# Kernel optimization log

Hardware: AMD Instinct MI355X
Metric: run time of the kernel (lower is better)

## Reference

```python
import jax, jax.numpy as jnp
import numpy as np

N, K, F_IN, F_HID, F_OUT = 500000, 16, 7, 40, 3

def setup_inputs() -> dict:
    key = jax.random.key(0)
    k1, k2, k3 = jax.random.split(key, 3)
    mailbox = jax.random.normal(k1, (N, K, F_IN), dtype=jnp.float32)
    W1 = jax.random.normal(k2, (F_IN, F_HID), dtype=jnp.float32) * (1.0 / np.sqrt(F_IN))
    b1 = jnp.zeros((F_HID,), dtype=jnp.float32)
    W2 = jax.random.normal(k3, (F_HID, F_OUT), dtype=jnp.float32) * (1.0 / np.sqrt(F_HID))
    b2 = jnp.zeros((F_OUT,), dtype=jnp.float32)
    return {"mailbox": mailbox, "W1": W1, "b1": b1, "W2": W2, "b2": b2}

def reference(mailbox, W1, b1, W2, b2):
    # MLP 7->40->3 applied per (node, neighbor) message, then mean over neighbors.
    h = jax.nn.relu(jnp.einsum('nkf,fh->nkh', mailbox, W1) + b1)  # [N,K,40]
    y = jnp.einsum('nkh,ho->nko', h, W2) + b2                     # [N,K,3]
    return jnp.mean(y, axis=1)                                    # [N,3]
```

## Files before the change

kernel.cpp:

```cpp
#include <hip/hip_runtime.h>
#include <stdint.h>

#define N_NODES 500000
#define K_NB 16
#define F_IN 7
#define F_HID 40
#define F_OUT 3
#define NODE_FLOATS (K_NB * F_IN)
#define NPW 16
#define WPB 4
#define NPB (NPW * WPB)

typedef __attribute__((address_space(3))) void lds_void_t;
typedef __attribute__((address_space(1))) const void glb_void_t;

__global__ __launch_bounds__(256) void aggre_kernel(
    const float* __restrict__ mailbox,
    const float* __restrict__ W1,
    const float* __restrict__ b1,
    const float* __restrict__ W2,
    const float* __restrict__ b2,
    float* __restrict__ out)
{
    __shared__ float4 w1lds[F_HID * 2];
    __shared__ float4 w2lds[F_HID];
    __shared__ __align__(16) float tile[WPB][NPW * NODE_FLOATS];

    const int t = threadIdx.x;
    if (t < F_HID * 2) {
        const int h = t >> 1;
        float4 v;
        if ((t & 1) == 0) {
            v.x = W1[0 * F_HID + h]; v.y = W1[1 * F_HID + h];
            v.z = W1[2 * F_HID + h]; v.w = W1[3 * F_HID + h];
        } else {
            v.x = W1[4 * F_HID + h]; v.y = W1[5 * F_HID + h];
            v.z = W1[6 * F_HID + h]; v.w = b1[h];
        }
        w1lds[t] = v;
    } else if (t < F_HID * 3) {
        const int h = t - F_HID * 2;
        float4 v;
        v.x = W2[h * F_OUT + 0];
        v.y = W2[h * F_OUT + 1];
        v.z = W2[h * F_OUT + 2];
        v.w = 0.0f;
        w2lds[h] = v;
    }
    __syncthreads();

    const int wave = t >> 6;
    const int lane = t & 63;
    const long tile0 = (long)blockIdx.x * NPB + (long)wave * NPW;
    if (tile0 >= N_NODES) return;

    const float* gsrc = mailbox + (size_t)tile0 * NODE_FLOATS;
    #pragma unroll
    for (int j = 0; j < 7; ++j) {
        const float* g = gsrc + (size_t)(j * 64 + lane) * 4;
        __builtin_amdgcn_global_load_lds(
            (glb_void_t*)g,
            (lds_void_t*)&tile[wave][j * 256],
            16, 0, 0);
    }
    __builtin_amdgcn_s_waitcnt(0x0f70);

    const int nloc = lane >> 2;
    const int r = lane & 3;
    const float* mp = &tile[wave][nloc * NODE_FLOATS + r * 28];
    float m[28];
    #pragma unroll
    for (int i = 0; i < 7; ++i) {
        const float4 v = ((const float4*)mp)[i];
        m[4 * i + 0] = v.x; m[4 * i + 1] = v.y;
        m[4 * i + 2] = v.z; m[4 * i + 3] = v.w;
    }

    float a0 = 0.0f, a1 = 0.0f, a2 = 0.0f;
    #pragma unroll 2
    for (int h = 0; h < F_HID; ++h) {
        const float4 wa = w1lds[2 * h + 0];
        const float4 wb = w1lds[2 * h + 1];
        float sh = 0.0f;
        #pragma unroll
        for (int kk = 0; kk < 4; ++kk) {
            const int o = kk * F_IN;
            float acc = wb.w;
            acc = fmaf(m[o + 0], wa.x, acc);
            acc = fmaf(m[o + 1], wa.y, acc);
            acc = fmaf(m[o + 2], wa.z, acc);
            acc = fmaf(m[o + 3], wa.w, acc);
            acc = fmaf(m[o + 4], wb.x, acc);
            acc = fmaf(m[o + 5], wb.y, acc);
            acc = fmaf(m[o + 6], wb.z, acc);
            sh += fmaxf(acc, 0.0f);
        }
        const float4 w2v = w2lds[h];
        a0 = fmaf(sh, w2v.x, a0);
        a1 = fmaf(sh, w2v.y, a1);
        a2 = fmaf(sh, w2v.z, a2);
    }

    a0 += __shfl_xor(a0, 1); a0 += __shfl_xor(a0, 2);
    a1 += __shfl_xor(a1, 1); a1 += __shfl_xor(a1, 2);
    a2 += __shfl_xor(a2, 1); a2 += __shfl_xor(a2, 2);

    if (r < F_OUT) {
        const float val = (r == 0) ? a0 : ((r == 1) ? a1 : a2);
        out[(size_t)(tile0 + nloc) * F_OUT + r] =
            fmaf(val, 1.0f / (float)K_NB, b2[r]);
    }
}

extern "C" void kernel_launch(void* const* d_in, const int* in_sizes, int n_in,
                              void* d_out, int out_size, void* d_ws, size_t ws_size,
                              hipStream_t stream) {
    const float* mailbox = (const float*)d_in[0];
    const float* W1      = (const float*)d_in[1];
    const float* b1      = (const float*)d_in[2];
    const float* W2      = (const float*)d_in[3];
    const float* b2      = (const float*)d_in[4];
    float* out = (float*)d_out;

    const int blocks = (N_NODES + NPB - 1) / NPB;
    aggre_kernel<<<blocks, 256, 0, stream>>>(mailbox, W1, b1, W2, b2, out);
}
```

Measured before the change: 315.4 us.

## Use packed v2f FMA math with a pre-duplicated weight table from a prep kernel

Adds a small prep kernel that writes W1, b1 and W2 into a workspace table, with each weight duplicated into float pairs. The main kernel reads these pairs through uniform global loads instead of staging weights in LDS behind a block barrier. The per-neighbor MLP is rewritten with two-wide vector FMAs so the compiler can emit packed FP32 instructions, processing two neighbors per operation and roughly halving VALU instruction count. The costs are an extra kernel launch, scalar-stride LDS reads for the messages, and weight reads that may become scalar or vector memory loads.

```diff
diff --git a/kernel.cpp b/kernel.cpp
--- a/kernel.cpp
+++ b/kernel.cpp
@@ -11,44 +11,53 @@
 #define WPB 4
 #define NPB (NPW * WPB)
 
+typedef float v2f __attribute__((ext_vector_type(2)));
+
 typedef __attribute__((address_space(3))) void lds_void_t;
 typedef __attribute__((address_space(1))) const void glb_void_t;
 
+__global__ void prep_kernel(const float* __restrict__ W1,
+                            const float* __restrict__ b1,
+                            const float* __restrict__ W2,
+                            const float* __restrict__ b2,
+                            float* __restrict__ ws)
+{
+    const int t = threadIdx.x;
+    if (t < F_HID) {
+        const int h = t;
+        float* p = ws + h * 16;
+        #pragma unroll
+        for (int i = 0; i < F_IN; ++i) {
+            const float w = W1[i * F_HID + h];
+            p[2 * i + 0] = w;
+            p[2 * i + 1] = w;
+        }
+        p[14] = b1[h];
+        p[15] = b1[h];
+    } else if (t < 2 * F_HID) {
+        const int h = t - F_HID;
+        float* p = ws + 40 * 16 + h * 8;
+        #pragma unroll
+        for (int c = 0; c < F_OUT; ++c) {
+            const float w = W2[h * F_OUT + c];
+            p[2 * c + 0] = w;
+            p[2 * c + 1] = w;
+        }
+        p[6] = 0.0f;
+        p[7] = 0.0f;
+    }
+}
+
 __global__ __launch_bounds__(256) void aggre_kernel(
     const float* __restrict__ mailbox,
-    const float* __restrict__ W1,
-    const float* __restrict__ b1,
-    const float* __restrict__ W2,
+    const float* __restrict__ wtab,
+    const float* __restrict__ w2tab,
     const float* __restrict__ b2,
     float* __restrict__ out)
 {
-    __shared__ float4 w1lds[F_HID * 2];
-    __shared__ float4 w2lds[F_HID];
     __shared__ __align__(16) float tile[WPB][NPW * NODE_FLOATS];
 
     const int t = threadIdx.x;
-    if (t < F_HID * 2) {
-        const int h = t >> 1;
-        float4 v;
-        if ((t & 1) == 0) {
-            v.x = W1[0 * F_HID + h]; v.y = W1[1 * F_HID + h];
-            v.z = W1[2 * F_HID + h]; v.w = W1[3 * F_HID + h];
-        } else {
-            v.x = W1[4 * F_HID + h]; v.y = W1[5 * F_HID + h];
-            v.z = W1[6 * F_HID + h]; v.w = b1[h];
-        }
-        w1lds[t] = v;
-    } else if (t < F_HID * 3) {
-        const int h = t - F_HID * 2;
-        float4 v;
-        v.x = W2[h * F_OUT + 0];
-        v.y = W2[h * F_OUT + 1];
-        v.z = W2[h * F_OUT + 2];
-        v.w = 0.0f;
-        w2lds[h] = v;
-    }
-    __syncthreads();
-
     const int wave = t >> 6;
     const int lane = t & 63;
     const long tile0 = (long)blockIdx.x * NPB + (long)wave * NPW;
@@ -67,46 +76,52 @@
 
     const int nloc = lane >> 2;
     const int r = lane & 3;
-    const float* mp = &tile[wave][nloc * NODE_FLOATS + r * 28];
-    float m[28];
+    const int base = nloc * NODE_FLOATS + r * 28;
+    v2f mA[F_IN], mB[F_IN];
     #pragma unroll
-    for (int i = 0; i < 7; ++i) {
-        const float4 v = ((const float4*)mp)[i];
-        m[4 * i + 0] = v.x; m[4 * i + 1] = v.y;
-        m[4 * i + 2] = v.z; m[4 * i + 3] = v.w;
+    for (int j = 0; j < F_IN; ++j) {
+        v2f a, b;
+        a.x = tile[wave][base + j];
+        a.y = tile[wave][base + 7 + j];
+        b.x = tile[wave][base + 14 + j];
+        b.y = tile[wave][base + 21 + j];
+        mA[j] = a;
+        mB[j] = b;
     }
 
-    float a0 = 0.0f, a1 = 0.0f, a2 = 0.0f;
-    #pragma unroll 2
+    const v2f* wt  = (const v2f*)wtab;
+    const v2f* w2t = (const v2f*)w2tab;
+
+    const v2f zero = {0.0f, 0.0f};
+    v2f a0 = zero, a1 = zero, a2 = zero;
+
+    #pragma unroll 4
     for (int h = 0; h < F_HID; ++h) {
-        const float4 wa = w1lds[2 * h + 0];
-        const float4 wb = w1lds[2 * h + 1];
-        float sh = 0.0f;
+        v2f accA = mA[0] * wt[h * 8 + 0];
+        v2f accB = mB[0] * wt[h * 8 + 0];
         #pragma unroll
-        for (int kk = 0; kk < 4; ++kk) {
-            const int o = kk * F_IN;
-            float acc = wb.w;
-            acc = fmaf(m[o + 0], wa.x, acc);
-            acc = fmaf(m[o + 1], wa.y, acc);
-            acc = fmaf(m[o + 2], wa.z, acc);
-            acc = fmaf(m[o + 3], wa.w, acc);
-            acc = fmaf(m[o + 4], wb.x, acc);
-            acc = fmaf(m[o + 5], wb.y, acc);
-            acc = fmaf(m[o + 6], wb.z, acc);
-            sh += fmaxf(acc, 0.0f);
+        for (int j = 1; j < F_IN; ++j) {
+            accA = __builtin_elementwise_fma(mA[j], wt[h * 8 + j], accA);
+            accB = __builtin_elementwise_fma(mB[j], wt[h * 8 + j], accB);
         }
-        const float4 w2v = w2lds[h];
-        a0 = fmaf(sh, w2v.x, a0);
-        a1 = fmaf(sh, w2v.y, a1);
-        a2 = fmaf(sh, w2v.z, a2);
+        const v2f bp = wt[h * 8 + 7];
+        accA = __builtin_elementwise_max(accA + bp, zero);
+        accB = __builtin_elementwise_max(accB + bp, zero);
+        const v2f sh = accA + accB;
+        a0 = __builtin_elementwise_fma(sh, w2t[h * 4 + 0], a0);
+        a1 = __builtin_elementwise_fma(sh, w2t[h * 4 + 1], a1);
+        a2 = __builtin_elementwise_fma(sh, w2t[h * 4 + 2], a2);
     }
 
-    a0 += __shfl_xor(a0, 1); a0 += __shfl_xor(a0, 2);
-    a1 += __shfl_xor(a1, 1); a1 += __shfl_xor(a1, 2);
-    a2 += __shfl_xor(a2, 1); a2 += __shfl_xor(a2, 2);
+    float s0 = a0.x + a0.y;
+    float s1 = a1.x + a1.y;
+    float s2 = a2.x + a2.y;
+    s0 += __shfl_xor(s0, 1); s0 += __shfl_xor(s0, 2);
+    s1 += __shfl_xor(s1, 1); s1 += __shfl_xor(s1, 2);
+    s2 += __shfl_xor(s2, 1); s2 += __shfl_xor(s2, 2);
 
     if (r < F_OUT) {
-        const float val = (r == 0) ? a0 : ((r == 1) ? a1 : a2);
+        const float val = (r == 0) ? s0 : ((r == 1) ? s1 : s2);
         out[(size_t)(tile0 + nloc) * F_OUT + r] =
             fmaf(val, 1.0f / (float)K_NB, b2[r]);
     }
@@ -120,8 +135,13 @@
     const float* b1      = (const float*)d_in[2];
     const float* W2      = (const float*)d_in[3];
     const float* b2      = (const float*)d_in[4];
+    float* ws  = (float*)d_ws;
     float* out = (float*)d_out;
 
+    prep_kernel<<<1, 128, 0, stream>>>(W1, b1, W2, b2, ws);
+
+    const float* wtab  = ws;
+    const float* w2tab = ws + 40 * 16;
     const int blocks = (N_NODES + NPB - 1) / NPB;
-    aggre_kernel<<<blocks, 256, 0, stream>>>(mailbox, W1, b1, W2, b2, out);
+    aggre_kernel<<<blocks, 256, 0, stream>>>(mailbox, wtab, w2tab, b2, out);
 }
```

New measurement: 320.3 us. About the same (+1.5%).
